# Performance work log

Measured on AMD Instinct MI355X. Metric: run time of the kernel, lower is better.

## Reference

```python
import jax, jax.numpy as jnp
import numpy as np

B, C, H, W = 4, 512, 64, 64
MID = C // 8  # 64


def setup_inputs() -> dict:
    key = jax.random.key(0)
    ks = jax.random.split(key, 8)
    s = 0.02
    return {
        "x": jax.random.normal(ks[0], (B, C, H, W), dtype=jnp.float32),
        "Wq": jax.random.normal(ks[1], (MID, C), dtype=jnp.float32) * s,
        "bq": jax.random.normal(ks[2], (MID,), dtype=jnp.float32) * s,
        "Wk": jax.random.normal(ks[3], (MID, C), dtype=jnp.float32) * s,
        "bk": jax.random.normal(ks[4], (MID,), dtype=jnp.float32) * s,
        "Wv": jax.random.normal(ks[5], (C, C), dtype=jnp.float32) * s,
        "bv": jax.random.normal(ks[6], (C,), dtype=jnp.float32) * s,
        "gamma": jax.random.uniform(ks[7], (1,), dtype=jnp.float32),
    }


def reference(x, Wq, bq, Wk, bk, Wv, bv, gamma):
    b, c, h, w = x.shape
    n = h * w
    xf = x.reshape(b, c, n)  # [B, C, N]
    # 1x1 convs are per-position linear maps
    q = jnp.einsum('mc,bcn->bnm', Wq, xf) + bq            # [B, N, mid]
    k = jnp.einsum('mc,bcn->bmn', Wk, xf) + bk[:, None]   # [B, mid, N]
    sim = jax.nn.softmax(jnp.einsum('bnm,bmj->bnj', q, k), axis=-1)  # [B, N, N]
    v = jnp.einsum('dc,bcn->bdn', Wv, xf) + bv[:, None]   # [B, C, N]
    # feat[:, d, i] = sum_j v[:, d, j] * sim[:, i, j]
    feat = jnp.einsum('bdj,bij->bdi', v, sim)             # [B, C, N]
    out = gamma[0] * feat + xf
    return out.reshape(b, c, h, w)
```

## Files before the change

kernel.cpp:

```cpp
#include <hip/hip_runtime.h>

#define BATCH 4
#define CCH   512
#define NN    4096
#define MIDD  64

typedef unsigned short u16;
typedef unsigned int   u32;
typedef short s8v  __attribute__((ext_vector_type(8)));
typedef float f16v __attribute__((ext_vector_type(16)));
typedef unsigned int u4v __attribute__((ext_vector_type(4)));

__device__ __forceinline__ u16 f2bf(float f) {
  u32 u = __float_as_uint(f);
  u += 0x7fffu + ((u >> 16) & 1u);
  return (u16)(u >> 16);
}

__device__ __forceinline__ void g2lds16(const u16* g, u16* l) {
  __builtin_amdgcn_global_load_lds(
      (const __attribute__((address_space(1))) u32*)(const void*)g,
      (__attribute__((address_space(3))) u32*)(void*)l, 16, 0, 0);
}

#define S_WAITCNT(vm, lgkm) \
  __builtin_amdgcn_s_waitcnt(((vm) & 15) | (((vm) >> 4) << 14) | (0x7 << 4) | ((lgkm) << 8))

__global__ __launch_bounds__(256) void prep_w(
    const float* __restrict__ Wq, const float* __restrict__ Wk,
    const float* __restrict__ Wv, u16* __restrict__ Wb)
{
  int e = (blockIdx.x * 256 + threadIdx.x) * 8;
  const float* src;
  if (e < 64 * 512)       src = Wq + e;
  else if (e < 128 * 512) src = Wk + (e - 64 * 512);
  else                    src = Wv + (e - 128 * 512);
  float4 v0 = *(const float4*)src;
  float4 v1 = *(const float4*)(src + 4);
  uint4 p;
  p.x = (u32)f2bf(v0.x) | ((u32)f2bf(v0.y) << 16);
  p.y = (u32)f2bf(v0.z) | ((u32)f2bf(v0.w) << 16);
  p.z = (u32)f2bf(v1.x) | ((u32)f2bf(v1.y) << 16);
  p.w = (u32)f2bf(v1.z) | ((u32)f2bf(v1.w) << 16);
  *(uint4*)(Wb + e) = p;
}

__global__ __launch_bounds__(256) void transpose_cast(
    const float* __restrict__ x, u16* __restrict__ xbT)
{
  const int b  = blockIdx.z;
  const int c0 = blockIdx.y * 64;
  const int n0 = blockIdx.x * 64;
  const int t  = threadIdx.x;
  __shared__ float ts[64 * 65];

  #pragma unroll
  for (int k = 0; k < 4; k++) {
    int idx = t + 256 * k;
    int cc = idx >> 4, n4 = idx & 15;
    float4 v = *(const float4*)&x[((size_t)(b * CCH + c0 + cc)) * NN + n0 + n4 * 4];
    float* p = &ts[cc * 65 + n4 * 4];
    p[0] = v.x; p[1] = v.y; p[2] = v.z; p[3] = v.w;
  }
  __syncthreads();

  const int n = t >> 2, cb = (t & 3) * 16;
  u16 tmp[16];
  #pragma unroll
  for (int j = 0; j < 16; j++) tmp[j] = f2bf(ts[(cb + j) * 65 + n]);
  u16* dst = &xbT[((size_t)b * NN + n0 + n) * CCH + c0 + cb];
  *(uint4*)&dst[0] = *(uint4*)&tmp[0];
  *(uint4*)&dst[8] = *(uint4*)&tmp[8];
}

__global__ __launch_bounds__(256, 2) void proj_gemm(
    const u16* __restrict__ xbT, const u16* __restrict__ Wb,
    const float* __restrict__ bq, const float* __restrict__ bk,
    const float* __restrict__ bv,
    u16* __restrict__ qT, u16* __restrict__ kT, u16* __restrict__ vF)
{
  const int b  = blockIdx.z;
  const int mt = blockIdx.y;
  const int n0 = blockIdx.x * 256;
  const int t  = threadIdx.x;
  const int ln = t & 31, hi = (t & 63) >> 5, w = t >> 6;
  const int l  = t & 63;
  const int l2 = l & 3, lr = l >> 2;
  const int swc = (l2 ^ (lr & 3)) * 8;

  const int mrow0 = (mt < 8) ? (128 + mt * 64) : ((mt == 8) ? 0 : 64);
  const float* bias = (mt < 8) ? (bv + mt * 64) : ((mt == 8) ? bq : bk);

  __shared__ u16 ws[2][64 * 32];
  __shared__ u16 xs[2][256 * 32];

  const u16* xsrc = xbT + ((size_t)b * NN + n0 + w * 64 + lr) * CCH + swc;
  const u16* wsrc = Wb + (size_t)(mrow0 + w * 16 + lr) * 512 + swc;

  f16v acc[4];
  #pragma unroll
  for (int i = 0; i < 4; i++)
    #pragma unroll
    for (int r = 0; r < 16; r++) acc[i][r] = 0.f;

  #pragma unroll
  for (int i = 0; i < 4; i++)
    g2lds16(xsrc + (size_t)(16 * i) * CCH, &xs[0][(w * 64 + i * 16) * 32]);
  g2lds16(wsrc, &ws[0][w * 16 * 32]);

  for (int it = 0; it < 16; it++) {
    const int cur = it & 1, nxt = cur ^ 1;
    __builtin_amdgcn_s_barrier();
    const int c1 = ((it + 1) & 15) * 32;
    #pragma unroll
    for (int i = 0; i < 4; i++)
      g2lds16(xsrc + (size_t)(16 * i) * CCH + c1, &xs[nxt][(w * 64 + i * 16) * 32]);
    g2lds16(wsrc + c1, &ws[nxt][w * 16 * 32]);

    S_WAITCNT(5, 15);
    __builtin_amdgcn_s_barrier();

    #pragma unroll
    for (int ks = 0; ks < 2; ks++) {
      const int cb = ((2 * ks + hi) ^ (ln & 3)) << 3;
      s8v a0 = *(const s8v*)&ws[cur][(ln)           * 32 + cb];
      s8v a1 = *(const s8v*)&ws[cur][(32 + ln)      * 32 + cb];
      s8v b0 = *(const s8v*)&xs[cur][(w * 64 + ln)      * 32 + cb];
      s8v b1 = *(const s8v*)&xs[cur][(w * 64 + 32 + ln) * 32 + cb];
      acc[0] = __builtin_amdgcn_mfma_f32_32x32x16_bf16(a0, b0, acc[0], 0, 0, 0);
      acc[1] = __builtin_amdgcn_mfma_f32_32x32x16_bf16(a0, b1, acc[1], 0, 0, 0);
      acc[2] = __builtin_amdgcn_mfma_f32_32x32x16_bf16(a1, b0, acc[2], 0, 0, 0);
      acc[3] = __builtin_amdgcn_mfma_f32_32x32x16_bf16(a1, b1, acc[3], 0, 0, 0);
    }
  }

  S_WAITCNT(0, 0);
  __builtin_amdgcn_s_barrier();

  if (mt < 8) {
    u16* xt = &xs[0][0];
    #pragma unroll
    for (int mi = 0; mi < 2; mi++)
      #pragma unroll
      for (int ni = 0; ni < 2; ni++) {
        f16v& a = acc[mi * 2 + ni];
        #pragma unroll
        for (int r = 0; r < 16; r++) {
          int row = (r & 3) + 8 * (r >> 2) + 4 * hi;
          int m   = mi * 32 + row;
          int nr  = w * 64 + ni * 32 + ln;
          int c8  = nr >> 3;
          xt[m * 256 + ((c8 ^ (m & 31)) << 3) + (nr & 7)] = f2bf(a[r] + bias[m]);
        }
      }
    __syncthreads();
    const int jt0 = n0 >> 6;
    const size_t dgb = ((size_t)b * 64 + jt0 + w) * 16 + mt * 2;
    #pragma unroll
    for (int mh = 0; mh < 2; mh++)
      #pragma unroll
      for (int ks = 0; ks < 4; ks++) {
        int c8 = w * 8 + ks * 2 + hi;
        int m  = mh * 32 + ln;
        s8v vv = *(const s8v*)&xt[m * 256 + ((c8 ^ ln) << 3)];
        *(s8v*)&vF[(((dgb + mh) * 4 + ks) * 64 + l) * 8] = vv;
      }
  } else {
    u16* dst = (mt == 8) ? qT : kT;
    u16* xt  = &xs[0][0];
    #pragma unroll
    for (int mi = 0; mi < 2; mi++)
      #pragma unroll
      for (int ni = 0; ni < 2; ni++) {
        f16v& a = acc[mi * 2 + ni];
        #pragma unroll
        for (int r = 0; r < 16; r++) {
          int row = (r & 3) + 8 * (r >> 2) + 4 * hi;
          int m   = mi * 32 + row;
          int nr  = w * 64 + ni * 32 + ln;
          xt[(nr << 6) + (((m >> 3) ^ (ln & 7)) << 3) + (m & 7)] = f2bf(a[r] + bias[m]);
        }
      }
    __syncthreads();
    const int r7 = t & 7;
    u16* drow = &dst[((size_t)b * NN + n0 + t) * 64];
    #pragma unroll
    for (int k = 0; k < 8; k++)
      *(uint4*)&drow[k * 8] = *(uint4*)&xt[(t << 6) + ((k ^ r7) << 3)];
  }
}

__global__ __launch_bounds__(256, 2) void attn_kernel(
    const u16* __restrict__ qT,
    const u16* __restrict__ kT,
    const u16* __restrict__ vF,
    const float* __restrict__ x,
    const float* __restrict__ gamma,
    float* __restrict__ out)
{
  __shared__ u16 ksm[3][64 * 64];

  const int bx    = blockIdx.x;
  const int slot  = bx & 7;
  const int b     = slot >> 1;
  const int dbase = (slot & 1) * 256;
  const int i0    = (bx >> 3) * 64;
  const int t     = threadIdx.x;
  const int l     = t & 63, ln = l & 31, hi = l >> 5;
  const int w     = t >> 6;
  const int qh    = w & 1;
  const int dh    = w >> 1;
  const int l3    = l & 7, lh3 = l >> 3;
  const int sw8   = (l3 ^ lh3) * 8;

  s8v qfrag[4];
  {
    const u16* qp = qT + ((size_t)b * NN + i0 + qh * 32 + ln) * 64 + hi * 8;
    #pragma unroll
    for (int k = 0; k < 4; k++) qfrag[k] = *(const s8v*)(qp + 16 * k);
  }

  const u16* ksrc = kT + (size_t)b * NN * 64 + (size_t)(16 * w + lh3) * 64 + sw8;
  const u16* vfb = vF + (size_t)b * (64 * 16 * 4 * 64 * 8);
  const int dgbase = (slot & 1) * 8 + dh * 4;

  f16v oacc[4];
  #pragma unroll
  for (int i = 0; i < 4; i++)
    #pragma unroll
    for (int r = 0; r < 16; r++) oacc[i][r] = 0.f;
  float lsum = 0.f;

  #pragma unroll
  for (int i = 0; i < 2; i++)
    g2lds16(ksrc + (size_t)(8 * i) * 64, &ksm[0][(w * 2 + i) * 512]);
  #pragma unroll
  for (int i = 0; i < 2; i++)
    g2lds16(ksrc + (size_t)(64 + 8 * i) * 64, &ksm[1][(w * 2 + i) * 512]);

  int cur = 0, nx1 = 1, nx2 = 2;
  for (int it = 0; it < 64; it++) {
    s8v vf[4][4];
    {
      const u16* vp = vfb + (size_t)(it * 16 + dgbase) * 2048 + l * 8;
      #pragma unroll
      for (int dgi = 0; dgi < 4; dgi++)
        #pragma unroll
        for (int ks = 0; ks < 4; ks++)
          vf[dgi][ks] = *(const s8v*)(vp + dgi * 2048 + ks * 512);
    }

    S_WAITCNT(16, 15);
    __builtin_amdgcn_s_barrier();

    {
      const int j2 = ((it + 2) & 63) * 64;
      u16* kdst = &ksm[0][0] + nx2 * 4096 + (w * 2) * 512;
      #pragma unroll
      for (int i = 0; i < 2; i++)
        g2lds16(ksrc + (size_t)(j2 + 8 * i) * 64, kdst + i * 512);
    }

    const u16* kcur = &ksm[0][0] + cur * 4096;
    f16v ssw[2];
    #pragma unroll
    for (int jh2 = 0; jh2 < 2; jh2++) {
      #pragma unroll
      for (int r = 0; r < 16; r++) ssw[jh2][r] = 0.f;
      #pragma unroll
      for (int ks = 0; ks < 4; ks++) {
        s8v kf = *(const s8v*)&kcur[(jh2 * 32 + ln) * 64 + (((2 * ks + hi) ^ l3) << 3)];
        ssw[jh2] = __builtin_amdgcn_mfma_f32_32x32x16_bf16(kf, qfrag[ks], ssw[jh2], 0, 0, 0);
      }
    }

    u4v pfq[4];
    #pragma unroll
    for (int a2 = 0; a2 < 2; a2++) {
      float pe[16];
      #pragma unroll
      for (int r = 0; r < 16; r++) {
        pe[r] = __expf(ssw[a2][r]);
        lsum += pe[r];
      }
      #pragma unroll
      for (int b2 = 0; b2 < 2; b2++)
        #pragma unroll
        for (int wd = 0; wd < 2; wd++) {
          u32 X, Y;
          asm("v_cvt_pk_bf16_f32 %0, %1, %2"
              : "=v"(X) : "v"(pe[8 * b2 + 2 * wd]), "v"(pe[8 * b2 + 2 * wd + 1]));
          asm("v_cvt_pk_bf16_f32 %0, %1, %2"
              : "=v"(Y) : "v"(pe[8 * b2 + 4 + 2 * wd]), "v"(pe[8 * b2 + 4 + 2 * wd + 1]));
          u32 T = hi ? X : Y;
          u32 R = (u32)__shfl_xor((int)T, 32);
          pfq[a2 * 2 + b2][wd]     = hi ? R : X;
          pfq[a2 * 2 + b2][wd + 2] = hi ? Y : R;
        }
    }

    #pragma unroll
    for (int ks = 0; ks < 4; ks++) {
      s8v pb = (s8v)pfq[ks];
      oacc[0] = __builtin_amdgcn_mfma_f32_32x32x16_bf16(vf[0][ks], pb, oacc[0], 0, 0, 0);
      oacc[1] = __builtin_amdgcn_mfma_f32_32x32x16_bf16(vf[1][ks], pb, oacc[1], 0, 0, 0);
      oacc[2] = __builtin_amdgcn_mfma_f32_32x32x16_bf16(vf[2][ks], pb, oacc[2], 0, 0, 0);
      oacc[3] = __builtin_amdgcn_mfma_f32_32x32x16_bf16(vf[3][ks], pb, oacc[3], 0, 0, 0);
    }

    int tmp = cur; cur = nx1; nx1 = nx2; nx2 = tmp;
  }

  S_WAITCNT(0, 0);

  const float lt   = lsum + __shfl_xor(lsum, 32);
  const float linv = 1.0f / lt;
  const float g0   = gamma[0];
  const int   q    = i0 + qh * 32 + ln;
  #pragma unroll
  for (int dgi = 0; dgi < 4; dgi++) {
    f16v& a = oacc[dgi];
    #pragma unroll
    for (int r = 0; r < 16; r++) {
      int dl = dh * 128 + dgi * 32 + (r & 3) + 8 * (r >> 2) + 4 * hi;
      size_t idx = ((size_t)b * CCH + dbase + dl) * NN + q;
      out[idx] = g0 * a[r] * linv + x[idx];
    }
  }
}

extern "C" void kernel_launch(void* const* d_in, const int* in_sizes, int n_in,
                              void* d_out, int out_size, void* d_ws, size_t ws_size,
                              hipStream_t stream) {
  const float* x     = (const float*)d_in[0];
  const float* Wq    = (const float*)d_in[1];
  const float* bq    = (const float*)d_in[2];
  const float* Wk    = (const float*)d_in[3];
  const float* bk    = (const float*)d_in[4];
  const float* Wv    = (const float*)d_in[5];
  const float* bv    = (const float*)d_in[6];
  const float* gamma = (const float*)d_in[7];
  float* out = (float*)d_out;

  u16* qT  = (u16*)d_ws;
  u16* kT  = qT  + (size_t)BATCH * NN * MIDD;
  u16* vF  = kT  + (size_t)BATCH * NN * MIDD;
  u16* xbT = vF  + (size_t)BATCH * CCH * NN;
  u16* Wb  = xbT + (size_t)BATCH * NN * CCH;

  prep_w<<<dim3(160), 256, 0, stream>>>(Wq, Wk, Wv, Wb);
  transpose_cast<<<dim3(NN / 64, CCH / 64, BATCH), 256, 0, stream>>>(x, xbT);
  proj_gemm<<<dim3(NN / 256, 10, BATCH), 256, 0, stream>>>(
      xbT, Wb, bq, bk, bv, qT, kT, vF);
  attn_kernel<<<dim3(512), 256, 0, stream>>>(qT, kT, vF, x, gamma, out);
}
```

Measured before the change: 239.8 us.

## Split QK^T score work across wave pairs and fold log2e into Wq for exp2

Each wave now computes only half of the 64 key scores per tile, selected by dh, instead of all 64. The two waves that share the same queries swap their bf16 probability fragments through a double-buffered LDS exchange with a barrier, and the row sums are combined through LDS at the end. This halves the redundant QK^T MFMA and exp work per wave. log2(e) is folded into Wq and bq during preprocessing so the softmax can use the native exp2 instruction instead of __expf. In exchange, every iteration gets an extra LDS round-trip and a block-wide barrier.

```diff
diff --git a/kernel.cpp b/kernel.cpp
--- a/kernel.cpp
+++ b/kernel.cpp
@@ -10,6 +10,8 @@
 typedef short s8v  __attribute__((ext_vector_type(8)));
 typedef float f16v __attribute__((ext_vector_type(16)));
 typedef unsigned int u4v __attribute__((ext_vector_type(4)));
+
+#define L2E 1.44269504088896340736f
 
 __device__ __forceinline__ u16 f2bf(float f) {
   u32 u = __float_as_uint(f);
@@ -32,16 +34,17 @@
 {
   int e = (blockIdx.x * 256 + threadIdx.x) * 8;
   const float* src;
-  if (e < 64 * 512)       src = Wq + e;
+  float sc = 1.0f;
+  if (e < 64 * 512)       { src = Wq + e; sc = L2E; }
   else if (e < 128 * 512) src = Wk + (e - 64 * 512);
   else                    src = Wv + (e - 128 * 512);
   float4 v0 = *(const float4*)src;
   float4 v1 = *(const float4*)(src + 4);
   uint4 p;
-  p.x = (u32)f2bf(v0.x) | ((u32)f2bf(v0.y) << 16);
-  p.y = (u32)f2bf(v0.z) | ((u32)f2bf(v0.w) << 16);
-  p.z = (u32)f2bf(v1.x) | ((u32)f2bf(v1.y) << 16);
-  p.w = (u32)f2bf(v1.z) | ((u32)f2bf(v1.w) << 16);
+  p.x = (u32)f2bf(sc * v0.x) | ((u32)f2bf(sc * v0.y) << 16);
+  p.y = (u32)f2bf(sc * v0.z) | ((u32)f2bf(sc * v0.w) << 16);
+  p.z = (u32)f2bf(sc * v1.x) | ((u32)f2bf(sc * v1.y) << 16);
+  p.w = (u32)f2bf(sc * v1.z) | ((u32)f2bf(sc * v1.w) << 16);
   *(uint4*)(Wb + e) = p;
 }
 
@@ -90,6 +93,7 @@
 
   const int mrow0 = (mt < 8) ? (128 + mt * 64) : ((mt == 8) ? 0 : 64);
   const float* bias = (mt < 8) ? (bv + mt * 64) : ((mt == 8) ? bq : bk);
+  const float bsc = (mt == 8) ? L2E : 1.0f;
 
   __shared__ u16 ws[2][64 * 32];
   __shared__ u16 xs[2][256 * 32];
@@ -178,7 +182,7 @@
           int row = (r & 3) + 8 * (r >> 2) + 4 * hi;
           int m   = mi * 32 + row;
           int nr  = w * 64 + ni * 32 + ln;
-          xt[(nr << 6) + (((m >> 3) ^ (ln & 7)) << 3) + (m & 7)] = f2bf(a[r] + bias[m]);
+          xt[(nr << 6) + (((m >> 3) ^ (ln & 7)) << 3) + (m & 7)] = f2bf(a[r] + bsc * bias[m]);
         }
       }
     __syncthreads();
@@ -199,6 +203,7 @@
     float* __restrict__ out)
 {
   __shared__ u16 ksm[3][64 * 64];
+  __shared__ u4v pex[2][512];
 
   const int bx    = blockIdx.x;
   const int slot  = bx & 7;
@@ -262,58 +267,70 @@
     }
 
     const u16* kcur = &ksm[0][0] + cur * 4096;
-    f16v ssw[2];
-    #pragma unroll
-    for (int jh2 = 0; jh2 < 2; jh2++) {
-      #pragma unroll
-      for (int r = 0; r < 16; r++) ssw[jh2][r] = 0.f;
-      #pragma unroll
-      for (int ks = 0; ks < 4; ks++) {
-        s8v kf = *(const s8v*)&kcur[(jh2 * 32 + ln) * 64 + (((2 * ks + hi) ^ l3) << 3)];
-        ssw[jh2] = __builtin_amdgcn_mfma_f32_32x32x16_bf16(kf, qfrag[ks], ssw[jh2], 0, 0, 0);
+    f16v ssw;
+    #pragma unroll
+    for (int r = 0; r < 16; r++) ssw[r] = 0.f;
+    #pragma unroll
+    for (int ks = 0; ks < 4; ks++) {
+      s8v kf = *(const s8v*)&kcur[(dh * 32 + ln) * 64 + (((2 * ks + hi) ^ l3) << 3)];
+      ssw = __builtin_amdgcn_mfma_f32_32x32x16_bf16(kf, qfrag[ks], ssw, 0, 0, 0);
+    }
+
+    float pe[16];
+    #pragma unroll
+    for (int r = 0; r < 16; r++) {
+      pe[r] = __builtin_amdgcn_exp2f(ssw[r]);
+      lsum += pe[r];
+    }
+    u4v own[2];
+    #pragma unroll
+    for (int b2 = 0; b2 < 2; b2++)
+      #pragma unroll
+      for (int wd = 0; wd < 2; wd++) {
+        u32 X, Y;
+        asm("v_cvt_pk_bf16_f32 %0, %1, %2"
+            : "=v"(X) : "v"(pe[8 * b2 + 2 * wd]), "v"(pe[8 * b2 + 2 * wd + 1]));
+        asm("v_cvt_pk_bf16_f32 %0, %1, %2"
+            : "=v"(Y) : "v"(pe[8 * b2 + 4 + 2 * wd]), "v"(pe[8 * b2 + 4 + 2 * wd + 1]));
+        u32 T = hi ? X : Y;
+        u32 R = (u32)__shfl_xor((int)T, 32);
+        own[b2][wd]     = hi ? R : X;
+        own[b2][wd + 2] = hi ? Y : R;
       }
-    }
-
-    u4v pfq[4];
-    #pragma unroll
-    for (int a2 = 0; a2 < 2; a2++) {
-      float pe[16];
-      #pragma unroll
-      for (int r = 0; r < 16; r++) {
-        pe[r] = __expf(ssw[a2][r]);
-        lsum += pe[r];
-      }
-      #pragma unroll
-      for (int b2 = 0; b2 < 2; b2++)
-        #pragma unroll
-        for (int wd = 0; wd < 2; wd++) {
-          u32 X, Y;
-          asm("v_cvt_pk_bf16_f32 %0, %1, %2"
-              : "=v"(X) : "v"(pe[8 * b2 + 2 * wd]), "v"(pe[8 * b2 + 2 * wd + 1]));
-          asm("v_cvt_pk_bf16_f32 %0, %1, %2"
-              : "=v"(Y) : "v"(pe[8 * b2 + 4 + 2 * wd]), "v"(pe[8 * b2 + 4 + 2 * wd + 1]));
-          u32 T = hi ? X : Y;
-          u32 R = (u32)__shfl_xor((int)T, 32);
-          pfq[a2 * 2 + b2][wd]     = hi ? R : X;
-          pfq[a2 * 2 + b2][wd + 2] = hi ? Y : R;
-        }
-    }
-
-    #pragma unroll
-    for (int ks = 0; ks < 4; ks++) {
-      s8v pb = (s8v)pfq[ks];
-      oacc[0] = __builtin_amdgcn_mfma_f32_32x32x16_bf16(vf[0][ks], pb, oacc[0], 0, 0, 0);
-      oacc[1] = __builtin_amdgcn_mfma_f32_32x32x16_bf16(vf[1][ks], pb, oacc[1], 0, 0, 0);
-      oacc[2] = __builtin_amdgcn_mfma_f32_32x32x16_bf16(vf[2][ks], pb, oacc[2], 0, 0, 0);
-      oacc[3] = __builtin_amdgcn_mfma_f32_32x32x16_bf16(vf[3][ks], pb, oacc[3], 0, 0, 0);
+
+    const int pc = it & 1;
+    pex[pc][(w * 2 + 0) * 64 + l] = own[0];
+    pex[pc][(w * 2 + 1) * 64 + l] = own[1];
+    S_WAITCNT(63, 0);
+    __builtin_amdgcn_s_barrier();
+    u4v o0 = pex[pc][((w ^ 2) * 2 + 0) * 64 + l];
+    u4v o1 = pex[pc][((w ^ 2) * 2 + 1) * 64 + l];
+
+    s8v pb0 = (s8v)(dh ? o0 : own[0]);
+    s8v pb1 = (s8v)(dh ? o1 : own[1]);
+    s8v pb2 = (s8v)(dh ? own[0] : o0);
+    s8v pb3 = (s8v)(dh ? own[1] : o1);
+
+    #pragma unroll
+    for (int dgi = 0; dgi < 4; dgi++) {
+      oacc[dgi] = __builtin_amdgcn_mfma_f32_32x32x16_bf16(vf[dgi][0], pb0, oacc[dgi], 0, 0, 0);
+      oacc[dgi] = __builtin_amdgcn_mfma_f32_32x32x16_bf16(vf[dgi][1], pb1, oacc[dgi], 0, 0, 0);
+      oacc[dgi] = __builtin_amdgcn_mfma_f32_32x32x16_bf16(vf[dgi][2], pb2, oacc[dgi], 0, 0, 0);
+      oacc[dgi] = __builtin_amdgcn_mfma_f32_32x32x16_bf16(vf[dgi][3], pb3, oacc[dgi], 0, 0, 0);
     }
 
     int tmp = cur; cur = nx1; nx1 = nx2; nx2 = tmp;
   }
 
   S_WAITCNT(0, 0);
-
-  const float lt   = lsum + __shfl_xor(lsum, 32);
+  __builtin_amdgcn_s_barrier();
+
+  float lw = lsum + __shfl_xor(lsum, 32);
+  float* lred = (float*)&pex[0][0];
+  if (hi == 0) lred[w * 32 + ln] = lw;
+  S_WAITCNT(63, 0);
+  __builtin_amdgcn_s_barrier();
+  const float lt   = lred[w * 32 + ln] + lred[(w ^ 2) * 32 + ln];
   const float linv = 1.0f / lt;
   const float g0   = gamma[0];
   const int   q    = i0 + qh * 32 + ln;
```

New measurement: 231.2 us. 3.6% less time.
